# Performance work log

Hardware: AMD Instinct MI355X
Metric: run time of the kernel (lower is better)

Reference implementation:

```python
import jax, jax.numpy as jnp
import numpy as np

EMBED_DIM = 1152
NUM_HEADS = 16
PROJ_SIZE = 1152
HEAD_DIM = PROJ_SIZE // NUM_HEADS  # 72
SEQ = 16384
N_SEG = 8
SEG_LEN = SEQ // N_SEG


def setup_inputs() -> dict:
    key = jax.random.key(0)
    ks = jax.random.split(key, 6)
    hidden_states = jax.random.normal(ks[0], (1, SEQ, EMBED_DIM), dtype=jnp.float32)
    qkv_w = jax.random.normal(ks[1], (3 * PROJ_SIZE, EMBED_DIM), dtype=jnp.float32) * 0.02
    qkv_b = jax.random.normal(ks[2], (3 * PROJ_SIZE,), dtype=jnp.float32) * 0.02
    out_w = jax.random.normal(ks[3], (EMBED_DIM, PROJ_SIZE), dtype=jnp.float32) * 0.02
    out_b = jax.random.normal(ks[4], (EMBED_DIM,), dtype=jnp.float32) * 0.02
    # rotary frequencies (seq, head_dim/2), full-head-dim rotary since 2*36 == 72
    rotary_pos_emb = jax.random.uniform(ks[5], (SEQ, HEAD_DIM // 2), dtype=jnp.float32) * 6.2831853
    cu_seqlens = jnp.arange(N_SEG + 1, dtype=jnp.int32) * SEG_LEN
    return {
        "hidden_states": hidden_states,
        "qkv_w": qkv_w,
        "qkv_b": qkv_b,
        "out_w": out_w,
        "out_b": out_b,
        "rotary_pos_emb": rotary_pos_emb,
        "cu_seqlens": cu_seqlens,
    }


def _rotate_half(x):
    x1, x2 = jnp.split(x, 2, axis=-1)
    return jnp.concatenate([-x2, x1], axis=-1)


def _apply_rope(x, cos, sin):
    # x: (b, s, h, d); cos/sin: (s, d) broadcast over batch and heads
    cos = cos[None, :, None, :]
    sin = sin[None, :, None, :]
    return x * cos + _rotate_half(x) * sin


def _forward(hidden_states, qkv_w, qkv_b, out_w, out_b, rotary_pos_emb, cu):
    b, s, _ = hidden_states.shape
    x = jnp.swapaxes(hidden_states, 0, 1)          # (s, b, embed)
    qkv = x @ qkv_w.T + qkv_b                      # (s, b, 3*proj)
    q, k, v = jnp.split(qkv, 3, axis=-1)
    def to_bshd(t):
        t = t.reshape(s, b, NUM_HEADS, HEAD_DIM)
        return jnp.swapaxes(t, 0, 1)               # (b, s, h, d)
    q, k, v = to_bshd(q), to_bshd(k), to_bshd(v)

    # rotary: cos/sin (s, d/2) -> (s, d) via non-interleaved repeat '(2 d)'
    cos = jnp.cos(rotary_pos_emb)
    sin = jnp.sin(rotary_pos_emb)
    cos2 = jnp.concatenate([cos, cos], axis=-1)    # (s, d)
    sin2 = jnp.concatenate([sin, sin], axis=-1)
    q = _apply_rope(q, cos2, sin2)
    k = _apply_rope(k, cos2, sin2)

    # block-diagonal (varlen) attention per cu_seqlens segment
    scale = 1.0 / np.sqrt(HEAD_DIM)
    outs = []
    for i in range(len(cu) - 1):
        s0, s1 = int(cu[i]), int(cu[i + 1])
        qi, ki, vi = q[:, s0:s1], k[:, s0:s1], v[:, s0:s1]   # (b, L, h, d)
        scores = jnp.einsum('bqhd,bkhd->bhqk', qi, ki) * scale
        attn = jax.nn.softmax(scores, axis=-1)
        outs.append(jnp.einsum('bhqk,bkhd->bqhd', attn, vi))
    ctx = jnp.concatenate(outs, axis=1)            # (b, s, h, d)
    ctx = jnp.swapaxes(ctx, 0, 1).reshape(s, b, PROJ_SIZE)  # (s, b, proj)
    out = ctx @ out_w.T + out_b                    # (s, b, embed)
    return jnp.swapaxes(out, 0, 1)                 # (b, s, embed)


def reference(hidden_states, qkv_w, qkv_b, out_w, out_b, rotary_pos_emb, cu_seqlens):
    cu = np.asarray(cu_seqlens)  # static segment boundaries
    return _forward(hidden_states, qkv_w, qkv_b, out_w, out_b, rotary_pos_emb, cu)
```

## Files before the change

### kernel.cpp

```cpp
#include <hip/hip_runtime.h>
#include <hip/hip_bf16.h>
#include <cstdint>

#define SEQ   16384
#define ED    1152
#define NH    16
#define HD    72
#define NSEG  8
#define SEGLEN 2048
#define QKVN  3456
#define NT    (SEGLEN / 64)

typedef __bf16 bf16x8 __attribute__((ext_vector_type(8)));
typedef float  f32x4  __attribute__((ext_vector_type(4)));
typedef __hip_bfloat16 bf16;

__device__ __forceinline__ unsigned short f2bfbits(float f) {
  bf16 h = __float2bfloat16(f);
  return __builtin_bit_cast(unsigned short, h);
}

__device__ __forceinline__ float fexp2(float x) {
#if __has_builtin(__builtin_amdgcn_exp2f)
  return __builtin_amdgcn_exp2f(x);
#else
  return exp2f(x);
#endif
}

__device__ __forceinline__ void gload_lds16(const void* g, void* l) {
  __builtin_amdgcn_global_load_lds(
      (__attribute__((address_space(1))) void*)(void*)g,
      (__attribute__((address_space(3))) void*)l, 16, 0, 0);
}

__global__ __launch_bounds__(256) void cvt_f32_bf16(const float* __restrict__ in,
                                                    bf16* __restrict__ out, int n4) {
  int i = blockIdx.x * 256 + threadIdx.x;
  if (i >= n4) return;
  float4 v = reinterpret_cast<const float4*>(in)[i];
  ushort4 o;
  o.x = f2bfbits(v.x); o.y = f2bfbits(v.y); o.z = f2bfbits(v.z); o.w = f2bfbits(v.w);
  reinterpret_cast<ushort4*>(out)[i] = o;
}

__global__ __launch_bounds__(256) void gemm_bt(const bf16* __restrict__ A,
                                               const bf16* __restrict__ B,
                                               const float* __restrict__ bias,
                                               void* __restrict__ Cout,
                                               int M, int N, int K, int out_bf16) {
  __shared__ __align__(16) bf16 As[128 * 32];
  __shared__ __align__(16) bf16 Bs[128 * 32];
  const int nt   = N >> 7;
  const int nwg  = gridDim.x;
  const int cpx  = nwg >> 3;
  const int bid  = blockIdx.x;
  const int swz  = (bid & 7) * cpx + (bid >> 3);
  const int bm   = swz / nt;
  const int bn   = swz % nt;
  const int tid  = threadIdx.x;
  const int lane = tid & 63;
  const int wave = tid >> 6;
  const int wr   = wave >> 1, wc = wave & 1;

  const bf16* Ab = A + (size_t)(bm * 128) * K;
  const bf16* Bb = B + (size_t)(bn * 128) * K;
  const int r0 = tid >> 2;
  const int c0 = (tid & 3) << 3;

  char* AsB = (char*)As;
  char* BsB = (char*)Bs;
  const int ldsoff = wave * 1024;

  const int row15 = lane & 15;
  const int koff  = (lane >> 4) << 3;

  f32x4 acc[4][4] = {};

  for (int k0 = 0; k0 < K; k0 += 32) {
    gload_lds16(Ab + (size_t)r0 * K + k0 + c0,        AsB + ldsoff);
    gload_lds16(Ab + (size_t)(r0 + 64) * K + k0 + c0, AsB + 4096 + ldsoff);
    gload_lds16(Bb + (size_t)r0 * K + k0 + c0,        BsB + ldsoff);
    gload_lds16(Bb + (size_t)(r0 + 64) * K + k0 + c0, BsB + 4096 + ldsoff);
    __syncthreads();
    bf16x8 a[4], b[4];
#pragma unroll
    for (int mi = 0; mi < 4; ++mi)
      a[mi] = *reinterpret_cast<const bf16x8*>(&As[(wr * 64 + mi * 16 + row15) * 32 + koff]);
#pragma unroll
    for (int ni = 0; ni < 4; ++ni)
      b[ni] = *reinterpret_cast<const bf16x8*>(&Bs[(wc * 64 + ni * 16 + row15) * 32 + koff]);
#pragma unroll
    for (int mi = 0; mi < 4; ++mi)
#pragma unroll
      for (int ni = 0; ni < 4; ++ni)
        acc[mi][ni] = __builtin_amdgcn_mfma_f32_16x16x32_bf16(a[mi], b[ni], acc[mi][ni], 0, 0, 0);
    __syncthreads();
  }

  const int crow = bm * 128 + wr * 64 + (lane >> 4) * 4;
  const int ccol = bn * 128 + wc * 64 + row15;
#pragma unroll
  for (int mi = 0; mi < 4; ++mi)
#pragma unroll
    for (int ni = 0; ni < 4; ++ni) {
      const int col = ccol + ni * 16;
      const float bv = bias[col];
#pragma unroll
      for (int r = 0; r < 4; ++r) {
        const int row = crow + mi * 16 + r;
        float v = acc[mi][ni][r] + bv;
        if (out_bf16)
          reinterpret_cast<bf16*>(Cout)[(size_t)row * N + col] = __float2bfloat16(v);
        else
          reinterpret_cast<float*>(Cout)[(size_t)row * N + col] = v;
      }
    }
}

__global__ __launch_bounds__(256) void rope_inplace(bf16* __restrict__ qkv,
                                                    const float* __restrict__ ang) {
  const int s = blockIdx.x;
  bf16* row = qkv + (size_t)s * QKVN;
  for (int i = threadIdx.x; i < 2 * NH * 36; i += 256) {
    int t   = i / (NH * 36);
    int rem = i - t * (NH * 36);
    int h   = rem / 36;
    int d2  = rem - h * 36;
    float a  = ang[s * 36 + d2];
    float cs = cosf(a), sn = sinf(a);
    bf16* p = row + t * ED + h * HD + d2;
    float x1 = __bfloat162float(p[0]);
    float x2 = __bfloat162float(p[36]);
    p[0]  = __float2bfloat16(x1 * cs - x2 * sn);
    p[36] = __float2bfloat16(x2 * cs + x1 * sn);
  }
}

__global__ __launch_bounds__(256, 4) void attn(const bf16* __restrict__ qkv,
                                               bf16* __restrict__ ctx) {
  const int blk  = blockIdx.x;
  const int qt   = (blk >> 3) & 15;
  const int g    = (((blk >> 7) & 15) << 3) | (blk & 7);
  const int head = g & 15;
  const int seg  = g >> 4;
  const int q0   = seg * SEGLEN + qt * 128;

  const int tid = threadIdx.x, lane = tid & 63, w = tid >> 6;
  const int row15 = lane & 15, hi = lane >> 4, koff = hi << 3;

  __shared__ __align__(16) bf16 Ks[64 * 72];
  __shared__ __align__(16) bf16 Vt[80 * 72];
  __shared__ __align__(16) bf16 Ps[128 * 72];

  const bf16* Qg = qkv + (size_t)q0 * QKVN + head * HD;
  const bf16* Kg = qkv + (size_t)(seg * SEGLEN) * QKVN + ED + head * HD;
  const bf16* Vg = qkv + (size_t)(seg * SEGLEN) * QKVN + 2 * ED + head * HD;

  {
    const bf16 one  = __float2bfloat16(1.0f);
    const bf16 zerob = __float2bfloat16(0.0f);
    for (int e = tid; e < 8 * 72; e += 256)
      Vt[72 * 72 + e] = (e < 72) ? one : zerob;
  }

  const bf16x8 zero8 = {};
  bf16x8 aq[2][3];
#pragma unroll
  for (int m = 0; m < 2; ++m) {
    const bf16* qrow = Qg + (size_t)(w * 32 + m * 16 + row15) * QKVN;
    aq[m][0] = *reinterpret_cast<const bf16x8*>(qrow + koff);
    aq[m][1] = *reinterpret_cast<const bf16x8*>(qrow + 32 + koff);
    aq[m][2] = (hi == 0) ? *reinterpret_cast<const bf16x8*>(qrow + 64) : zero8;
  }

  f32x4 oacc[2][5] = {};
  const float c2 = 0.11785113019775793f * 1.4426950408889634f;

  auto stage_k = [&](int kt2) {
    const bf16* Kt = Kg + (size_t)kt2 * 64 * QKVN;
    char* KsB = (char*)Ks;
    for (int gq = w; gq < 9; gq += 4) {
      int chunk = gq * 64 + lane;
      int row = chunk / 9;
      int cc  = chunk - row * 9;
      gload_lds16(Kt + (size_t)row * QKVN + cc * 8, KsB + gq * 1024);
    }
  };

  auto stage_v = [&](int kt2) {
    const bf16* src0 = Vg + (size_t)kt2 * 64 * QKVN;
    for (int c = tid; c < 576; c += 256) {
      int j = c / 9, m9 = c - j * 9;
      int d0 = m9 << 3;
      int jj = (j + (m9 << 3)) & 63;
      bf16x8 v = *reinterpret_cast<const bf16x8*>(src0 + (size_t)j * QKVN + d0);
      const unsigned short* u = reinterpret_cast<const unsigned short*>(&v);
#pragma unroll
      for (int e = 0; e < 8; ++e)
        Vt[(d0 + e) * 72 + jj] = __builtin_bit_cast(bf16, u[e]);
    }
  };

  auto qkt_soft = [&]() {
    f32x4 s[2][4] = {};
    __builtin_amdgcn_s_setprio(1);
#pragma unroll
    for (int ks = 0; ks < 2; ++ks) {
#pragma unroll
      for (int n = 0; n < 4; ++n) {
        bf16x8 bk = *reinterpret_cast<const bf16x8*>(&Ks[(n * 16 + row15) * 72 + ks * 32 + koff]);
        s[0][n] = __builtin_amdgcn_mfma_f32_16x16x32_bf16(aq[0][ks], bk, s[0][n], 0, 0, 0);
        s[1][n] = __builtin_amdgcn_mfma_f32_16x16x32_bf16(aq[1][ks], bk, s[1][n], 0, 0, 0);
      }
    }
#pragma unroll
    for (int n = 0; n < 4; ++n) {
      bf16x8 bk = (hi == 0) ? *reinterpret_cast<const bf16x8*>(&Ks[(n * 16 + row15) * 72 + 64]) : zero8;
      s[0][n] = __builtin_amdgcn_mfma_f32_16x16x32_bf16(aq[0][2], bk, s[0][n], 0, 0, 0);
      s[1][n] = __builtin_amdgcn_mfma_f32_16x16x32_bf16(aq[1][2], bk, s[1][n], 0, 0, 0);
    }
    __builtin_amdgcn_s_setprio(0);
    const int prow_base = w * 32 + hi * 4;
#pragma unroll
    for (int m = 0; m < 2; ++m)
#pragma unroll
      for (int n = 0; n < 4; ++n)
#pragma unroll
        for (int r = 0; r < 4; ++r) {
          float p = fexp2(fmaf(s[m][n][r], c2, -4.0f));
          Ps[(prow_base + m * 16 + r) * 72 + n * 16 + row15] =
              __builtin_bit_cast(bf16, f2bfbits(p));
        }
  };

  auto pv = [&]() {
    __builtin_amdgcn_s_setprio(1);
#pragma unroll
    for (int ks = 0; ks < 2; ++ks) {
      bf16x8 ap0 = *reinterpret_cast<const bf16x8*>(&Ps[(w * 32 + row15) * 72 + ks * 32 + koff]);
      bf16x8 ap1 = *reinterpret_cast<const bf16x8*>(&Ps[(w * 32 + 16 + row15) * 72 + ks * 32 + koff]);
#pragma unroll
      for (int n = 0; n < 5; ++n) {
        const int vrow = n * 16 + row15;
        const int col = (ks * 32 + (hi << 3) + ((vrow >> 3) << 3)) & 63;
        bf16x8 bv = *reinterpret_cast<const bf16x8*>(&Vt[vrow * 72 + col]);
        oacc[0][n] = __builtin_amdgcn_mfma_f32_16x16x32_bf16(ap0, bv, oacc[0][n], 0, 0, 0);
        oacc[1][n] = __builtin_amdgcn_mfma_f32_16x16x32_bf16(ap1, bv, oacc[1][n], 0, 0, 0);
      }
    }
    __builtin_amdgcn_s_setprio(0);
  };

  stage_k(0);
  stage_v(0);
  for (int kt = 0; kt < NT; ++kt) {
    __syncthreads();
    qkt_soft();
    pv();
    __syncthreads();
    if (kt + 1 < NT) {
      stage_k(kt + 1);
      stage_v(kt + 1);
    }
  }

#pragma unroll
  for (int m = 0; m < 2; ++m) {
#pragma unroll
    for (int r = 0; r < 4; ++r) {
      float l = __shfl(oacc[m][4][r], (lane & 48) + 8);
      float inv = 1.0f / l;
#pragma unroll
      for (int n = 0; n < 5; ++n) {
        const int d = n * 16 + row15;
        if (d < HD) {
          const int row = q0 + w * 32 + m * 16 + hi * 4 + r;
          ctx[(size_t)row * ED + head * HD + d] = __float2bfloat16(oacc[m][n][r] * inv);
        }
      }
    }
  }
}

extern "C" void kernel_launch(void* const* d_in, const int* in_sizes, int n_in,
                              void* d_out, int out_size, void* d_ws, size_t ws_size,
                              hipStream_t stream) {
  const float* hidden = (const float*)d_in[0];
  const float* qkv_w  = (const float*)d_in[1];
  const float* qkv_b  = (const float*)d_in[2];
  const float* out_w  = (const float*)d_in[3];
  const float* out_b  = (const float*)d_in[4];
  const float* rope   = (const float*)d_in[5];

  const size_t SZ_QKV = (size_t)SEQ * QKVN * 2;
  const size_t SZ_X   = (size_t)SEQ * ED * 2;
  const size_t SZ_W   = (size_t)QKVN * ED * 2;
  const size_t NEED   = SZ_QKV + SZ_X + SZ_W;
  if (ws_size < NEED) return;

  char* ws = (char*)d_ws;
  bf16* qkvbf = (bf16*)(ws);
  bf16* Xbf   = (bf16*)(ws + SZ_QKV);
  bf16* Wbf   = (bf16*)(ws + SZ_QKV + SZ_X);

  cvt_f32_bf16<<<(SEQ * ED / 4 + 255) / 256, 256, 0, stream>>>(hidden, Xbf, SEQ * ED / 4);
  cvt_f32_bf16<<<(QKVN * ED / 4 + 255) / 256, 256, 0, stream>>>(qkv_w, Wbf, QKVN * ED / 4);

  gemm_bt<<<(SEQ / 128) * (QKVN / 128), 256, 0, stream>>>(Xbf, Wbf, qkv_b, qkvbf,
                                                          SEQ, QKVN, ED, 1);

  cvt_f32_bf16<<<(ED * ED / 4 + 255) / 256, 256, 0, stream>>>(out_w, Wbf, ED * ED / 4);

  rope_inplace<<<SEQ, 256, 0, stream>>>(qkvbf, rope);

  attn<<<NSEG * NH * (SEGLEN / 128), 256, 0, stream>>>(qkvbf, Xbf);

  gemm_bt<<<(SEQ / 128) * (ED / 128), 256, 0, stream>>>(Xbf, Wbf, out_b, d_out,
                                                        SEQ, ED, ED, 0);
}
```

Baseline: 576.7 us.

## Pre-transpose V into global layout and stage it via async LDS loads

Adds a transpose_v kernel that writes V once per head into a transposed, swizzled global buffer, including the ones and zero padding rows used for the softmax row sum. The attention kernel then stages V tiles with direct global-to-LDS 16-byte loads instead of transposing element-wise into shared memory on every key tile. This removes the repeated per-block scalar LDS transpose, since each V tile was previously transposed by all 16 query tiles. The cost is an extra kernel launch, a workspace buffer of about 42 MB, and an extra pass over V through global memory.

```diff
diff --git a/kernel.cpp b/kernel.cpp
--- a/kernel.cpp
+++ b/kernel.cpp
@@ -10,6 +10,7 @@
 #define SEGLEN 2048
 #define QKVN  3456
 #define NT    (SEGLEN / 64)
+#define VTROWS 80
 
 typedef __bf16 bf16x8 __attribute__((ext_vector_type(8)));
 typedef float  f32x4  __attribute__((ext_vector_type(4)));
@@ -137,7 +138,51 @@
   }
 }
 
+__global__ __launch_bounds__(256, 4) void transpose_v(const bf16* __restrict__ qkv,
+                                                      bf16* __restrict__ vt) {
+  const int h  = blockIdx.x & 15;
+  const int st = blockIdx.x >> 4;
+  const int s0 = st * 64;
+  const int tid = threadIdx.x;
+  __shared__ __align__(16) bf16 Lt[72 * 72];
+
+  const bf16* src = qkv + (size_t)s0 * QKVN + 2 * ED + h * HD;
+  for (int c = tid; c < 576; c += 256) {
+    int j = c / 9, m9 = c - j * 9;
+    int d0 = m9 << 3;
+    int jj = (j + (m9 << 3)) & 63;
+    bf16x8 v = *reinterpret_cast<const bf16x8*>(src + (size_t)j * QKVN + d0);
+    const unsigned short* u = reinterpret_cast<const unsigned short*>(&v);
+#pragma unroll
+    for (int e = 0; e < 8; ++e)
+      Lt[(d0 + e) * 72 + jj] = __builtin_bit_cast(bf16, u[e]);
+  }
+  __syncthreads();
+
+  bf16x8 ones8, zero8 = {};
+  {
+    unsigned short ob = f2bfbits(1.0f);
+#pragma unroll
+    for (int e = 0; e < 8; ++e) ones8[e] = __builtin_bit_cast(__bf16, ob);
+  }
+  bf16* dst = vt + (size_t)(h * VTROWS) * SEQ + s0;
+  for (int c = tid; c < VTROWS * 8; c += 256) {
+    int d = c >> 3, sc = c & 7;
+    bf16x8 v;
+    int og = sc;
+    if (d < 72) {
+      int col = (((sc + (d >> 3)) << 3)) & 63;
+      v = *reinterpret_cast<const bf16x8*>(&Lt[d * 72 + col]);
+      og = (sc + (d & 7)) & 7;
+    } else {
+      v = (d == 72) ? ones8 : zero8;
+    }
+    *reinterpret_cast<bf16x8*>(dst + (size_t)d * SEQ + (og << 3)) = v;
+  }
+}
+
 __global__ __launch_bounds__(256, 4) void attn(const bf16* __restrict__ qkv,
+                                               const bf16* __restrict__ vt,
                                                bf16* __restrict__ ctx) {
   const int blk  = blockIdx.x;
   const int qt   = (blk >> 3) & 15;
@@ -150,19 +195,12 @@
   const int row15 = lane & 15, hi = lane >> 4, koff = hi << 3;
 
   __shared__ __align__(16) bf16 Ks[64 * 72];
-  __shared__ __align__(16) bf16 Vt[80 * 72];
+  __shared__ __align__(16) bf16 Vt[VTROWS * 64];
   __shared__ __align__(16) bf16 Ps[128 * 72];
 
-  const bf16* Qg = qkv + (size_t)q0 * QKVN + head * HD;
-  const bf16* Kg = qkv + (size_t)(seg * SEGLEN) * QKVN + ED + head * HD;
-  const bf16* Vg = qkv + (size_t)(seg * SEGLEN) * QKVN + 2 * ED + head * HD;
-
-  {
-    const bf16 one  = __float2bfloat16(1.0f);
-    const bf16 zerob = __float2bfloat16(0.0f);
-    for (int e = tid; e < 8 * 72; e += 256)
-      Vt[72 * 72 + e] = (e < 72) ? one : zerob;
-  }
+  const bf16* Qg  = qkv + (size_t)q0 * QKVN + head * HD;
+  const bf16* Kg  = qkv + (size_t)(seg * SEGLEN) * QKVN + ED + head * HD;
+  const bf16* Vtg = vt + (size_t)(head * VTROWS) * SEQ + seg * SEGLEN;
 
   const bf16x8 zero8 = {};
   bf16x8 aq[2][3];
@@ -189,16 +227,12 @@
   };
 
   auto stage_v = [&](int kt2) {
-    const bf16* src0 = Vg + (size_t)kt2 * 64 * QKVN;
-    for (int c = tid; c < 576; c += 256) {
-      int j = c / 9, m9 = c - j * 9;
-      int d0 = m9 << 3;
-      int jj = (j + (m9 << 3)) & 63;
-      bf16x8 v = *reinterpret_cast<const bf16x8*>(src0 + (size_t)j * QKVN + d0);
-      const unsigned short* u = reinterpret_cast<const unsigned short*>(&v);
-#pragma unroll
-      for (int e = 0; e < 8; ++e)
-        Vt[(d0 + e) * 72 + jj] = __builtin_bit_cast(bf16, u[e]);
+    const bf16* Vsrc = Vtg + (size_t)kt2 * 64;
+    char* VsB = (char*)Vt;
+    for (int i = w; i < 10; i += 4) {
+      int c = i * 64 + lane;
+      int d = c >> 3, g8 = c & 7;
+      gload_lds16(Vsrc + (size_t)d * SEQ + g8 * 8, VsB + i * 1024);
     }
   };
 
@@ -243,8 +277,8 @@
 #pragma unroll
       for (int n = 0; n < 5; ++n) {
         const int vrow = n * 16 + row15;
-        const int col = (ks * 32 + (hi << 3) + ((vrow >> 3) << 3)) & 63;
-        bf16x8 bv = *reinterpret_cast<const bf16x8*>(&Vt[vrow * 72 + col]);
+        const int cA = ((((ks << 2) + hi + (vrow & 7)) & 7) << 3);
+        bf16x8 bv = *reinterpret_cast<const bf16x8*>(&Vt[vrow * 64 + (ks == 0 ? cA : cA)]);
         oacc[0][n] = __builtin_amdgcn_mfma_f32_16x16x32_bf16(ap0, bv, oacc[0][n], 0, 0, 0);
         oacc[1][n] = __builtin_amdgcn_mfma_f32_16x16x32_bf16(ap1, bv, oacc[1][n], 0, 0, 0);
       }
@@ -296,13 +330,15 @@
   const size_t SZ_QKV = (size_t)SEQ * QKVN * 2;
   const size_t SZ_X   = (size_t)SEQ * ED * 2;
   const size_t SZ_W   = (size_t)QKVN * ED * 2;
-  const size_t NEED   = SZ_QKV + SZ_X + SZ_W;
+  const size_t SZ_VT  = (size_t)NH * VTROWS * SEQ * 2;
+  const size_t NEED   = SZ_QKV + SZ_X + SZ_W + SZ_VT;
   if (ws_size < NEED) return;
 
   char* ws = (char*)d_ws;
   bf16* qkvbf = (bf16*)(ws);
   bf16* Xbf   = (bf16*)(ws + SZ_QKV);
   bf16* Wbf   = (bf16*)(ws + SZ_QKV + SZ_X);
+  bf16* vtb   = (bf16*)(ws + SZ_QKV + SZ_X + SZ_W);
 
   cvt_f32_bf16<<<(SEQ * ED / 4 + 255) / 256, 256, 0, stream>>>(hidden, Xbf, SEQ * ED / 4);
   cvt_f32_bf16<<<(QKVN * ED / 4 + 255) / 256, 256, 0, stream>>>(qkv_w, Wbf, QKVN * ED / 4);
@@ -314,7 +350,9 @@
 
   rope_inplace<<<SEQ, 256, 0, stream>>>(qkvbf, rope);
 
-  attn<<<NSEG * NH * (SEGLEN / 128), 256, 0, stream>>>(qkvbf, Xbf);
+  transpose_v<<<NH * (SEQ / 64), 256, 0, stream>>>(qkvbf, vtb);
+
+  attn<<<NSEG * NH * (SEGLEN / 128), 256, 0, stream>>>(qkvbf, vtb, Xbf);
 
   gemm_bt<<<(SEQ / 128) * (ED / 128), 256, 0, stream>>>(Xbf, Wbf, out_b, d_out,
                                                         SEQ, ED, ED, 0);
```

Result: faster. 558.2 us (-3.2%).
